# Kernel optimization log

Hardware: AMD Instinct MI355X
Metric: run time of the kernel (lower is better)

Reference implementation:

```python
import jax, jax.numpy as jnp
import numpy as np

B, S, A = 65536, 376, 17
H1, H2, K = 400, 300, 15
MAX_ACTION = 1.0


def setup_inputs() -> dict:
    key = jax.random.key(0)
    ks = jax.random.split(key, 16)

    def lin(kw, fan_in, fan_out):
        lim = 1.0 / np.sqrt(fan_in)
        k1, k2 = jax.random.split(kw)
        W = jax.random.uniform(k1, (fan_in, fan_out), jnp.float32, -lim, lim)
        b = jax.random.uniform(k2, (fan_out,), jnp.float32, -lim, lim)
        return W, b

    W1, b1 = lin(ks[0], S, H1)
    W2, b2 = lin(ks[1], H1, H2)
    Wmu, bmu = lin(ks[2], H2, A)
    Wlv, blv = lin(ks[3], H2, A)
    Wu, bu = lin(ks[4], H2, K * A)
    Ww, bw = lin(ks[5], H2, K * A)
    Wb, bb = lin(ks[6], H2, K)
    x = jax.random.normal(ks[7], (B, S), jnp.float32)
    eps = jax.random.normal(ks[8], (B, A), jnp.float32)
    return dict(x=x, eps=eps, W1=W1, b1=b1, W2=W2, b2=b2, Wmu=Wmu, bmu=bmu,
                Wlv=Wlv, blv=blv, Wu=Wu, bu=bu, Ww=Ww, bw=bw, Wb=Wb, bb=bb)


def _flow_chain(action, u, w, b):
    # u, w: (K, B, A); b: (K, B). Sequential planar flow -> lax.scan over K.
    def step(carry, uwb):
        z, ldj = carry
        u_k, w_k, b_k = uwb
        uw = jnp.sum(w_k * u_k, -1)                       # (B,)
        m_uw = -1.0 + jax.nn.softplus(uw)
        w_norm_sq = jnp.sum(w_k * w_k, -1)
        u_hat = u_k + ((m_uw - uw) / w_norm_sq)[:, None] * w_k  # invertibility reparam
        wzb = jnp.sum(w_k * z, -1) + b_k                  # (B,)
        t = jnp.tanh(wzb)
        z_new = z + u_hat * t[:, None]
        psi_u = jnp.sum(w_k * u_hat, -1) * (1.0 - t * t)  # psi^T u_hat
        ldj_new = ldj + jnp.log(jnp.abs(1.0 + psi_u))
        return (z_new, ldj_new), None

    init = (action, jnp.zeros(action.shape[0], action.dtype))
    (z_fin, ldj), _ = jax.lax.scan(step, init, (u, w, b))
    return z_fin, ldj


def reference(x, eps, W1, b1, W2, b2, Wmu, bmu, Wlv, blv, Wu, bu, Ww, bw, Wb, bb):
    h = jax.nn.relu(x @ W1 + b1)
    h = jax.nn.relu(h @ W2 + b2)
    mu = MAX_ACTION * jnp.tanh(h @ Wmu + bmu)
    log_var = MAX_ACTION * jnp.tanh(h @ Wlv + blv)
    std = jnp.exp(log_var)                 # torch code uses log_var.exp() as the scale
    action = mu + std * eps                # rsample

    u = (h @ Wu + bu).reshape(B, K, A).transpose(1, 0, 2)   # (K, B, A)
    w = (h @ Ww + bw).reshape(B, K, A).transpose(1, 0, 2)   # (K, B, A)
    b = (h @ Wb + bb).T                                      # (K, B)

    final_action, log_det_j = _flow_chain(action, u, w, b)

    # Normal(mu, std).log_prob(action) summed over action dim; (action-mu)/std == eps
    log_2pi = jnp.float32(np.log(2.0 * np.pi))
    log_prob = jnp.sum(-0.5 * eps * eps - log_var - 0.5 * log_2pi, axis=-1)
    log_prob_final = log_prob - log_det_j
    prob_final = jnp.exp(log_prob_final)
    return final_action, prob_final, log_prob_final
```

## Files before the change

kernel.cpp:

```cpp
#include <hip/hip_runtime.h>

typedef unsigned short ushort_t;
typedef unsigned int uint_t;
typedef __bf16 bf16x8 __attribute__((ext_vector_type(8)));
typedef float f32x4 __attribute__((ext_vector_type(4)));

#define B_ROWS 65536

#define KT1 12
#define NT1 30
#define KTC1 15
#define KI2 13
#define NT2 20
#define KTC2 10
#define KI3 10
#define NT3 40
#define LDH3 20

#define SZ1 (NT1 * KT1 * 512)
#define SZ2 (NT2 * KI2 * 512)
#define SZ3 (NT3 * KI3 * 512)

__device__ inline float bf2f(ushort_t u) {
    union { uint_t i; float f; } x; x.i = ((uint_t)u) << 16; return x.f;
}
__device__ inline ushort_t f2bf(float f) {
    uint_t u = __float_as_uint(f);
    return (ushort_t)((u + 0x7FFFu + ((u >> 16) & 1u)) >> 16);
}
__device__ inline uint_t pack2(float a, float b) {
    return (uint_t)f2bf(a) | ((uint_t)f2bf(b) << 16);
}
__device__ inline float fast_tanh(float x) {
    float e = __expf(2.f * x);
    return 1.f - 2.f / (e + 1.f);
}
__device__ inline void gl2lds16(const ushort_t* g, ushort_t* l) {
    __builtin_amdgcn_global_load_lds(
        (const __attribute__((address_space(1))) uint_t*)g,
        (__attribute__((address_space(3))) uint_t*)l, 16, 0, 0);
}

__global__ void pack_kernel(const float* __restrict__ W1, const float* __restrict__ W2,
                            const float* __restrict__ Wmu, const float* __restrict__ Wlv,
                            const float* __restrict__ Wu, const float* __restrict__ Ww,
                            const float* __restrict__ Wb,
                            const float* __restrict__ b1, const float* __restrict__ b2,
                            const float* __restrict__ bmu, const float* __restrict__ blv,
                            const float* __restrict__ bu, const float* __restrict__ bw,
                            const float* __restrict__ bb,
                            ushort_t* __restrict__ W1t, ushort_t* __restrict__ W2t,
                            ushort_t* __restrict__ Wht,
                            float* __restrict__ b1p, float* __restrict__ b2p,
                            float* __restrict__ bHp)
{
    int i = blockIdx.x * 256 + threadIdx.x;
    if (i < SZ1) {
        int t = i >> 9, pos = i & 511;
        int l = pos >> 3, j = pos & 7;
        int n = (t / KT1) * 16 + (l & 15);
        int k = (t % KT1) * 32 + (l >> 4) * 8 + j;
        W1t[i] = (n < 400 && k < 376) ? f2bf(W1[k * 400 + n]) : (ushort_t)0;
    } else if (i < SZ1 + SZ2) {
        int i2 = i - SZ1;
        int t = i2 >> 9, pos = i2 & 511;
        int l = pos >> 3, j = pos & 7;
        int n = (t / KI2) * 16 + (l & 15);
        int k = (t % KI2) * 32 + (l >> 4) * 8 + j;
        W2t[i2] = (n < 300 && k < 400) ? f2bf(W2[k * 300 + n]) : (ushort_t)0;
    } else if (i < SZ1 + SZ2 + SZ3) {
        int i3 = i - SZ1 - SZ2;
        int t = i3 >> 9, pos = i3 & 511;
        int l = pos >> 3, j = pos & 7;
        int n = (t / KI3) * 16 + (l & 15);
        int k = (t % KI3) * 32 + (l >> 4) * 8 + j;
        float v = 0.f;
        if (k < 300) {
            if      (n < 17)  v = Wmu[k * 17 + n];
            else if (n < 34)  v = Wlv[k * 17 + (n - 17)];
            else if (n < 289) v = Wu[k * 255 + (n - 34)];
            else if (n < 544) v = Ww[k * 255 + (n - 289)];
            else if (n < 559) v = Wb[k * 15 + (n - 544)];
        }
        Wht[i3] = f2bf(v);
    } else {
        int j = i - SZ1 - SZ2 - SZ3;
        if (j < 480) {
            b1p[j] = (j < 400) ? b1[j] : 0.f;
        } else if (j < 800) {
            int n = j - 480;
            b2p[n] = (n < 300) ? b2[n] : 0.f;
        } else if (j < 1440) {
            int n = j - 800;
            float v = 0.f;
            if      (n < 17)  v = bmu[n];
            else if (n < 34)  v = blv[n - 17];
            else if (n < 289) v = bu[n - 34];
            else if (n < 544) v = bw[n - 289];
            else if (n < 559) v = bb[n - 544];
            bHp[n] = v;
        }
    }
}

__global__ __launch_bounds__(256)
void cvt_kernel(const float* __restrict__ x, ushort_t* __restrict__ xt, int nUnits)
{
    int U = blockIdx.x * 256 + threadIdx.x;
    if (U >= nUnits) return;
    int t = U >> 6, l = U & 63;
    int rowblk = t / KT1, kblk = t - rowblk * KT1;
    long row = (long)rowblk * 16 + (l & 15);
    int k0 = kblk * 32 + (l >> 4) * 8;
    uint4 o = {0u, 0u, 0u, 0u};
    if (k0 + 8 <= 376) {
        const float4* p = reinterpret_cast<const float4*>(x + row * 376 + k0);
        float4 v0 = p[0], v1 = p[1];
        o.x = pack2(v0.x, v0.y); o.y = pack2(v0.z, v0.w);
        o.z = pack2(v1.x, v1.y); o.w = pack2(v1.z, v1.w);
    }
    reinterpret_cast<uint4*>(xt)[U] = o;
}

template<bool RELU, bool OUT_TILED>
__global__ __launch_bounds__(256)
void gemm_tile(const ushort_t* __restrict__ A, const ushort_t* __restrict__ Bt,
               const float* __restrict__ bias, ushort_t* __restrict__ C,
               int kTA, int kIters, int kTC)
{
    __shared__ ushort_t As[8 * 512];
    __shared__ ushort_t Bs[10 * 512];
    const int tid = threadIdx.x;
    const int lane = tid & 63, wv = tid >> 6;
    const int q = lane >> 4, l16 = lane & 15;
    const int nb0 = blockIdx.x * 10;
    const int rowblk0 = blockIdx.y * 8;

    f32x4 acc[2][10];
    #pragma unroll
    for (int r = 0; r < 2; ++r)
        #pragma unroll
        for (int c = 0; c < 10; ++c)
            acc[r][c] = (f32x4){0.f, 0.f, 0.f, 0.f};

    for (int kt = 0; kt < kIters; ++kt) {
        #pragma unroll
        for (int i = 0; i < 2; ++i) {
            int t = wv * 2 + i;
            gl2lds16(A + (((size_t)(rowblk0 + t) * kTA + kt) << 9) + lane * 8,
                     &As[t << 9]);
        }
        #pragma unroll
        for (int t2 = 0; t2 < 3; ++t2) {
            int t = wv + t2 * 4;
            if (t < 10)
                gl2lds16(Bt + (((size_t)(nb0 + t) * kIters + kt) << 9) + lane * 8,
                         &Bs[t << 9]);
        }
        __syncthreads();

        bf16x8 a0 = __builtin_bit_cast(bf16x8,
            *reinterpret_cast<const uint4*>(&As[((wv * 2 + 0) << 9) + lane * 8]));
        bf16x8 a1 = __builtin_bit_cast(bf16x8,
            *reinterpret_cast<const uint4*>(&As[((wv * 2 + 1) << 9) + lane * 8]));
        #pragma unroll
        for (int c = 0; c < 10; ++c) {
            bf16x8 b = __builtin_bit_cast(bf16x8,
                *reinterpret_cast<const uint4*>(&Bs[(c << 9) + lane * 8]));
            acc[0][c] = __builtin_amdgcn_mfma_f32_16x16x32_bf16(a0, b, acc[0][c], 0, 0, 0);
            acc[1][c] = __builtin_amdgcn_mfma_f32_16x16x32_bf16(a1, b, acc[1][c], 0, 0, 0);
        }
        __syncthreads();
    }

    #pragma unroll
    for (int r = 0; r < 2; ++r) {
        int rowblk = rowblk0 + wv * 2 + r;
        #pragma unroll
        for (int c = 0; c < 10; ++c) {
            int n = (nb0 + c) * 16 + l16;
            float bv = bias[n];
            #pragma unroll
            for (int reg = 0; reg < 4; ++reg) {
                float v = acc[r][c][reg] + bv;
                if (RELU) v = fmaxf(v, 0.f);
                int mrow = q * 4 + reg;
                if (OUT_TILED) {
                    size_t off = (((size_t)rowblk * kTC + (n >> 5)) << 9)
                               + (size_t)(((n >> 3) & 3) * 16 + mrow) * 8 + (n & 7);
                    C[off] = f2bf(v);
                } else {
                    long m = (long)rowblk * 16 + mrow;
                    C[m * (long)kTC + n] = f2bf(v);
                }
            }
        }
    }
}

__device__ inline void ld_group8(const ushort_t* hb, int g, float* dst) {
    uint4 v = *reinterpret_cast<const uint4*>(hb + ((g >> 2) << 9) + ((g & 3) << 7));
    uint_t q[4] = {v.x, v.y, v.z, v.w};
    #pragma unroll
    for (int m = 0; m < 4; ++m) {
        dst[2 * m]     = __uint_as_float(q[m] << 16);
        dst[2 * m + 1] = __uint_as_float(q[m] & 0xFFFF0000u);
    }
}

__global__ __launch_bounds__(64)
void flow_kernel(const ushort_t* __restrict__ heads, const float* __restrict__ eps,
                 float* __restrict__ out, int rowBase, int Btot)
{
    const int tid = threadIdx.x;
    const long row = (long)blockIdx.x * 64 + tid;
    const ushort_t* hb = heads + (((size_t)(row >> 4) * LDH3) << 9)
                               + (size_t)((row & 15) << 3);

    float z[17];
    float lp = 0.f;
    {
        float a[40];
        #pragma unroll
        for (int g = 0; g < 5; ++g) ld_group8(hb, g, &a[g * 8]);
        #pragma unroll
        for (int i = 0; i < 17; ++i) {
            float mu = fast_tanh(a[i]);
            float lv = fast_tanh(a[17 + i]);
            float ep = eps[row * 17 + i];
            z[i] = mu + __expf(lv) * ep;
            lp += -0.5f * ep * ep - lv - 0.918938533f;
        }
    }

    float bv[16];
    ld_group8(hb, 68, &bv[0]);
    ld_group8(hb, 69, &bv[8]);

    float ldj = 0.f;
    #pragma unroll
    for (int k = 0; k < 15; ++k) {
        const int su = 34 + 17 * k;
        const int sw = 289 + 17 * k;
        const int gu = su >> 3, ou = su & 7;
        const int gw = sw >> 3, ow = sw & 7;
        float au[24], aw[24];
        ld_group8(hb, gu + 0, &au[0]);
        ld_group8(hb, gu + 1, &au[8]);
        ld_group8(hb, gu + 2, &au[16]);
        ld_group8(hb, gw + 0, &aw[0]);
        ld_group8(hb, gw + 1, &aw[8]);
        ld_group8(hb, gw + 2, &aw[16]);

        float uw = 0.f, w2 = 0.f, wz = 0.f;
        #pragma unroll
        for (int i = 0; i < 17; ++i) {
            float wi = aw[ow + i], ui = au[ou + i];
            uw += wi * ui;
            w2 += wi * wi;
            wz += wi * z[i];
        }
        float sp = (uw > 15.f) ? uw : __logf(1.f + __expf(uw));
        float m = sp - 1.f;
        float coef = (m - uw) / fmaxf(w2, 1e-20f);
        float t = fast_tanh(wz + bv[k]);
        #pragma unroll
        for (int i = 0; i < 17; ++i)
            z[i] += (au[ou + i] + coef * aw[ow + i]) * t;
        float psi = m * (1.f - t * t);
        ldj += __logf(fmaxf(fabsf(1.f + psi), 1e-30f));
    }

    const long g = rowBase + row;
    #pragma unroll
    for (int i = 0; i < 17; ++i) out[g * 17 + i] = z[i];
    float lpf = lp - ldj;
    out[(long)Btot * 17 + g] = __expf(lpf);
    out[(long)Btot * 18 + g] = lpf;
}

extern "C" void kernel_launch(void* const* d_in, const int* in_sizes, int n_in,
                              void* d_out, int out_size, void* d_ws, size_t ws_size,
                              hipStream_t stream)
{
    const float* x   = (const float*)d_in[0];
    const float* eps = (const float*)d_in[1];
    float* out = (float*)d_out;

    const size_t wUS = (size_t)SZ1 + SZ2 + SZ3;
    const size_t fixedBytes = wUS * 2 + (480 + 320 + 640) * 4;
    int Mc = 2048;
    {
        const int cand[6] = {65536, 32768, 16384, 8192, 4096, 2048};
        for (int i = 0; i < 6; ++i) {
            size_t req = (size_t)cand[i] * 2048 + fixedBytes;
            if (req <= ws_size) { Mc = cand[i]; break; }
        }
    }

    ushort_t* region1 = (ushort_t*)d_ws;
    ushort_t* region2 = region1 + (size_t)Mc * 640;
    ushort_t* W1t = region2 + (size_t)Mc * 384;
    ushort_t* W2t = W1t + SZ1;
    ushort_t* Wht = W2t + SZ2;
    float* b1p = (float*)(Wht + SZ3);
    float* b2p = b1p + 480;
    float* bHp = b2p + 320;

    const int packN = SZ1 + SZ2 + SZ3 + 1440;
    pack_kernel<<<(packN + 255) / 256, 256, 0, stream>>>(
        (const float*)d_in[2],  (const float*)d_in[4],
        (const float*)d_in[6],  (const float*)d_in[8],
        (const float*)d_in[10], (const float*)d_in[12], (const float*)d_in[14],
        (const float*)d_in[3],  (const float*)d_in[5],
        (const float*)d_in[7],  (const float*)d_in[9],
        (const float*)d_in[11], (const float*)d_in[13], (const float*)d_in[15],
        W1t, W2t, Wht, b1p, b2p, bHp);

    const int nChunks = B_ROWS / Mc;
    const int nUnits = Mc * 48;
    for (int c = 0; c < nChunks; ++c) {
        const float* xc = x + (size_t)c * Mc * 376;
        cvt_kernel<<<(nUnits + 255) / 256, 256, 0, stream>>>(xc, region2, nUnits);
        gemm_tile<true, true><<<dim3(3, Mc / 128), 256, 0, stream>>>(
            region2, W1t, b1p, region1, KT1, KT1, KTC1);
        gemm_tile<true, true><<<dim3(2, Mc / 128), 256, 0, stream>>>(
            region1, W2t, b2p, region2, KTC1, KI2, KTC2);
        gemm_tile<false, true><<<dim3(4, Mc / 128), 256, 0, stream>>>(
            region2, Wht, bHp, region1, KTC2, KI3, LDH3);
        flow_kernel<<<Mc / 64, 64, 0, stream>>>(region1, eps + (size_t)c * Mc * 17,
                                                out, c * Mc, B_ROWS);
    }
}
```

Measured before the change: 381.2 us.

## Split flow chain across four lanes per row with padded head layout

Repacks the head GEMM output so each of mu, log_var, b and every u/w flow slot sits in its own 8-aligned group padded to 24 columns. The flow kernel then spreads each row over four threads, each holding eight action components, and combines the dot products with cross-lane shuffles. The goal is to cut per-thread register pressure and raise parallelism in the serial 15-step flow. In exchange the head GEMM grows from 640 to 800 output columns, with an extra column tile of wasted padding work and more workspace traffic, and the fourth lane of each row does no useful component work.

```diff
diff --git a/kernel.cpp b/kernel.cpp
--- a/kernel.cpp
+++ b/kernel.cpp
@@ -14,8 +14,9 @@
 #define NT2 20
 #define KTC2 10
 #define KI3 10
-#define NT3 40
-#define LDH3 20
+#define NT3 50
+#define LDH3 25
+
 
 #define SZ1 (NT1 * KT1 * 512)
 #define SZ2 (NT2 * KI2 * 512)
@@ -76,11 +77,14 @@
         int k = (t % KI3) * 32 + (l >> 4) * 8 + j;
         float v = 0.f;
         if (k < 300) {
-            if      (n < 17)  v = Wmu[k * 17 + n];
-            else if (n < 34)  v = Wlv[k * 17 + (n - 17)];
-            else if (n < 289) v = Wu[k * 255 + (n - 34)];
-            else if (n < 544) v = Ww[k * 255 + (n - 289)];
-            else if (n < 559) v = Wb[k * 15 + (n - 544)];
+            if (n < 24)      { if (n < 17) v = Wmu[k * 17 + n]; }
+            else if (n < 48) { int c = n - 24; if (c < 17) v = Wlv[k * 17 + c]; }
+            else if (n < 64) { int c = n - 48; if (c < 15) v = Wb[k * 15 + c]; }
+            else if (n < 784) {
+                int r = n - 64, slot = r / 48, c = r % 48;
+                if (c < 24) { if (c < 17) v = Wu[k * 255 + slot * 17 + c]; }
+                else        { int c2 = c - 24; if (c2 < 17) v = Ww[k * 255 + slot * 17 + c2]; }
+            }
         }
         Wht[i3] = f2bf(v);
     } else {
@@ -90,14 +94,17 @@
         } else if (j < 800) {
             int n = j - 480;
             b2p[n] = (n < 300) ? b2[n] : 0.f;
-        } else if (j < 1440) {
+        } else if (j < 1600) {
             int n = j - 800;
             float v = 0.f;
-            if      (n < 17)  v = bmu[n];
-            else if (n < 34)  v = blv[n - 17];
-            else if (n < 289) v = bu[n - 34];
-            else if (n < 544) v = bw[n - 289];
-            else if (n < 559) v = bb[n - 544];
+            if (n < 24)      { if (n < 17) v = bmu[n]; }
+            else if (n < 48) { int c = n - 24; if (c < 17) v = blv[c]; }
+            else if (n < 64) { int c = n - 48; if (c < 15) v = bb[c]; }
+            else if (n < 784) {
+                int r = n - 64, slot = r / 48, c = r % 48;
+                if (c < 24) { if (c < 17) v = bu[slot * 17 + c]; }
+                else        { int c2 = c - 24; if (c2 < 17) v = bw[slot * 17 + c2]; }
+            }
             bHp[n] = v;
         }
     }
@@ -208,75 +215,86 @@
     }
 }
 
-__global__ __launch_bounds__(64)
+__global__ __launch_bounds__(256, 4)
 void flow_kernel(const ushort_t* __restrict__ heads, const float* __restrict__ eps,
                  float* __restrict__ out, int rowBase, int Btot)
 {
     const int tid = threadIdx.x;
-    const long row = (long)blockIdx.x * 64 + tid;
+    const int sub = tid & 3;
+    const long row = (long)blockIdx.x * 64 + (tid >> 2);
     const ushort_t* hb = heads + (((size_t)(row >> 4) * LDH3) << 9)
                                + (size_t)((row & 15) << 3);
 
-    float z[17];
+    float z[8];
     float lp = 0.f;
     {
-        float a[40];
-        #pragma unroll
-        for (int g = 0; g < 5; ++g) ld_group8(hb, g, &a[g * 8]);
-        #pragma unroll
-        for (int i = 0; i < 17; ++i) {
-            float mu = fast_tanh(a[i]);
-            float lv = fast_tanh(a[17 + i]);
-            float ep = eps[row * 17 + i];
-            z[i] = mu + __expf(lv) * ep;
-            lp += -0.5f * ep * ep - lv - 0.918938533f;
+        float amu[8] = {0,0,0,0,0,0,0,0}, alv[8] = {0,0,0,0,0,0,0,0};
+        if (sub < 3) {
+            ld_group8(hb, sub, amu);
+            ld_group8(hb, 3 + sub, alv);
+        }
+        float ep[8];
+        #pragma unroll
+        for (int c = 0; c < 8; ++c) {
+            int i = sub * 8 + c;
+            ep[c] = (i < 17) ? eps[row * 17 + i] : 0.f;
+        }
+        #pragma unroll
+        for (int c = 0; c < 8; ++c) {
+            float mu = fast_tanh(amu[c]);
+            float lv = fast_tanh(alv[c]);
+            z[c] = mu + __expf(lv) * ep[c];
+            int i = sub * 8 + c;
+            lp += (i < 17) ? (-0.5f * ep[c] * ep[c] - lv - 0.918938533f) : 0.f;
         }
     }
 
     float bv[16];
-    ld_group8(hb, 68, &bv[0]);
-    ld_group8(hb, 69, &bv[8]);
+    ld_group8(hb, 6, &bv[0]);
+    ld_group8(hb, 7, &bv[8]);
 
     float ldj = 0.f;
     #pragma unroll
     for (int k = 0; k < 15; ++k) {
-        const int su = 34 + 17 * k;
-        const int sw = 289 + 17 * k;
-        const int gu = su >> 3, ou = su & 7;
-        const int gw = sw >> 3, ow = sw & 7;
-        float au[24], aw[24];
-        ld_group8(hb, gu + 0, &au[0]);
-        ld_group8(hb, gu + 1, &au[8]);
-        ld_group8(hb, gu + 2, &au[16]);
-        ld_group8(hb, gw + 0, &aw[0]);
-        ld_group8(hb, gw + 1, &aw[8]);
-        ld_group8(hb, gw + 2, &aw[16]);
-
+        float au[8] = {0,0,0,0,0,0,0,0}, aw[8] = {0,0,0,0,0,0,0,0};
+        if (sub < 3) {
+            ld_group8(hb, 8 + 6 * k + sub, au);
+            ld_group8(hb, 11 + 6 * k + sub, aw);
+        }
         float uw = 0.f, w2 = 0.f, wz = 0.f;
         #pragma unroll
-        for (int i = 0; i < 17; ++i) {
-            float wi = aw[ow + i], ui = au[ou + i];
-            uw += wi * ui;
-            w2 += wi * wi;
-            wz += wi * z[i];
-        }
+        for (int c = 0; c < 8; ++c) {
+            uw += aw[c] * au[c];
+            w2 += aw[c] * aw[c];
+            wz += aw[c] * z[c];
+        }
+        uw += __shfl_xor(uw, 1); uw += __shfl_xor(uw, 2);
+        w2 += __shfl_xor(w2, 1); w2 += __shfl_xor(w2, 2);
+        wz += __shfl_xor(wz, 1); wz += __shfl_xor(wz, 2);
+
         float sp = (uw > 15.f) ? uw : __logf(1.f + __expf(uw));
         float m = sp - 1.f;
         float coef = (m - uw) / fmaxf(w2, 1e-20f);
         float t = fast_tanh(wz + bv[k]);
         #pragma unroll
-        for (int i = 0; i < 17; ++i)
-            z[i] += (au[ou + i] + coef * aw[ow + i]) * t;
+        for (int c = 0; c < 8; ++c)
+            z[c] += (au[c] + coef * aw[c]) * t;
         float psi = m * (1.f - t * t);
         ldj += __logf(fmaxf(fabsf(1.f + psi), 1e-30f));
     }
 
+    lp += __shfl_xor(lp, 1); lp += __shfl_xor(lp, 2);
     const long g = rowBase + row;
     #pragma unroll
-    for (int i = 0; i < 17; ++i) out[g * 17 + i] = z[i];
+    for (int c = 0; c < 8; ++c) {
+        int i = sub * 8 + c;
+        if (i < 17) out[g * 17 + i] = z[c];
+    }
     float lpf = lp - ldj;
-    out[(long)Btot * 17 + g] = __expf(lpf);
-    out[(long)Btot * 18 + g] = lpf;
+    if (sub == 0) {
+        out[(long)Btot * 17 + g] = __expf(lpf);
+        out[(long)Btot * 18 + g] = lpf;
+    }
 }
 
 extern "C" void kernel_launch(void* const* d_in, const int* in_sizes, int n_in,
@@ -288,18 +306,18 @@
     float* out = (float*)d_out;
 
     const size_t wUS = (size_t)SZ1 + SZ2 + SZ3;
-    const size_t fixedBytes = wUS * 2 + (480 + 320 + 640) * 4;
+    const size_t fixedBytes = wUS * 2 + (480 + 320 + 800) * 4;
     int Mc = 2048;
     {
         const int cand[6] = {65536, 32768, 16384, 8192, 4096, 2048};
         for (int i = 0; i < 6; ++i) {
-            size_t req = (size_t)cand[i] * 2048 + fixedBytes;
+            size_t req = (size_t)cand[i] * 2368 + fixedBytes;
             if (req <= ws_size) { Mc = cand[i]; break; }
         }
     }
 
     ushort_t* region1 = (ushort_t*)d_ws;
-    ushort_t* region2 = region1 + (size_t)Mc * 640;
+    ushort_t* region2 = region1 + (size_t)Mc * 800;
     ushort_t* W1t = region2 + (size_t)Mc * 384;
     ushort_t* W2t = W1t + SZ1;
     ushort_t* Wht = W2t + SZ2;
@@ -307,7 +325,7 @@
     float* b2p = b1p + 480;
     float* bHp = b2p + 320;
 
-    const int packN = SZ1 + SZ2 + SZ3 + 1440;
+    const int packN = SZ1 + SZ2 + SZ3 + 1600;
     pack_kernel<<<(packN + 255) / 256, 256, 0, stream>>>(
         (const float*)d_in[2],  (const float*)d_in[4],
         (const float*)d_in[6],  (const float*)d_in[8],
@@ -326,9 +344,9 @@
             region2, W1t, b1p, region1, KT1, KT1, KTC1);
         gemm_tile<true, true><<<dim3(2, Mc / 128), 256, 0, stream>>>(
             region1, W2t, b2p, region2, KTC1, KI2, KTC2);
-        gemm_tile<false, true><<<dim3(4, Mc / 128), 256, 0, stream>>>(
+        gemm_tile<false, true><<<dim3(5, Mc / 128), 256, 0, stream>>>(
             region2, Wht, bHp, region1, KTC2, KI3, LDH3);
-        flow_kernel<<<Mc / 64, 64, 0, stream>>>(region1, eps + (size_t)c * Mc * 17,
-                                                out, c * Mc, B_ROWS);
-    }
-}
+        flow_kernel<<<Mc / 64, 256, 0, stream>>>(region1, eps + (size_t)c * Mc * 17,
+                                                 out, c * Mc, B_ROWS);
+    }
+}
```

Measured after the change: 366.5 us. 3.9% less time.
